# Performance work log

Hardware: AMD Instinct MI355X
Metric: run time of the kernel (lower is better)

The kernel has to match this reference:

```python
import jax, jax.numpy as jnp
from jax import lax
import numpy as np

CHUNK = 64


def short_conv(x, w):
    # depthwise causal conv1d: x (B,L,D), w (D,K)
    L = x.shape[1]
    K = w.shape[1]
    xp = jnp.pad(x, ((0, 0), (K - 1, 0), (0, 0)))
    return sum(xp[:, j:j + L, :] * w[:, j] for j in range(K))


def o2b_weighted_delta_rule(k, q, v, b):
    # k,q,v,b: (B,L,H,D) float32, zero initial state
    B, L, H, D = k.shape
    C = CHUNK
    Nc = L // C

    def to_chunks(t):  # (B,L,H,D) -> (Nc,B,H,C,D)
        return t.transpose(0, 2, 1, 3).reshape(B, H, Nc, C, D).transpose(2, 0, 1, 3, 4)

    Kc, Qc, Vc, Bc = map(to_chunks, (k, q, v, b))
    eyeC = jnp.eye(C, dtype=jnp.float32)
    W0 = jnp.zeros((B, H, D, D), jnp.float32)
    Cf = float(C)

    def step(carry, xs):
        W_t, W_avg = carry
        i, Ki, Qi, Vi, Bi = xs
        KiT = jnp.swapaxes(Ki, -1, -2)
        T = jnp.tril(Bi @ KiT, k=-1)                      # (B,H,C,C) strictly lower
        inv = jnp.linalg.inv(eyeC + T)
        Ui = inv @ (Vi - Bi @ W_t)                        # (B,H,C,D)
        W_new = W_t + KiT @ Ui
        ts = (i * C).astype(jnp.float32)                  # init t == 0 for all batches
        idx = jnp.arange(1, C + 1, dtype=jnp.float32) + ts  # (C,)
        cs = jnp.cumsum(idx)
        weighted_idx = idx + idx.sum() - cs
        w_i = (weighted_idx / ((1 + ts + Cf) * (ts + Cf) / 2))[:, None]  # (C,1)
        coef1 = ts / (ts + Cf) * ((1 + ts) / (1 + ts + Cf))
        coef2 = Cf / (ts + Cf) * ((ts * 2 + 1 + Cf) / (1 + ts + Cf))
        W_avg_new = coef1 * W_avg + coef2 * W_t + KiT @ (Ui * w_i)
        tri0 = (1 + ts) * ts / 2
        a = (tri0 / (tri0 + cs))[:, None]                 # (C,1)
        c = 1.0 - a
        r = cs[:, None]                                   # (C,1)
        j_idx = (cs - idx)[None, :]                       # (1,C)
        T_mat = jnp.where(r >= j_idx, (r - j_idx) / (tri0 + r), 0.0)  # (C,C)
        O_i = (Qi @ W_avg) * a + (Qi @ W_t) * c + (T_mat * (Qi @ KiT)) @ Ui
        return (W_new, W_avg_new), O_i

    (_, _), O = lax.scan(step, (W0, W0), (jnp.arange(Nc), Kc, Qc, Vc, Bc))
    # O: (Nc,B,H,C,D) -> (B,L,H,D)
    return O.transpose(1, 2, 0, 3, 4).reshape(B, H, L, D).transpose(0, 2, 1, 3)


def setup_inputs() -> dict:
    key = jax.random.key(0)
    ks = jax.random.split(key, 9)
    B, L, Dm, H = 4, 2048, 1024, 16
    Dh, K = Dm // H, 4
    s = 0.02
    return {
        'x': jax.random.normal(ks[0], (B, L, Dm), jnp.float32),
        'Wk': s * jax.random.normal(ks[1], (Dm, Dm), jnp.float32),
        'bk': jnp.zeros((Dm,), jnp.float32),
        'Wq': s * jax.random.normal(ks[2], (Dm, Dm), jnp.float32),
        'bq': jnp.zeros((Dm,), jnp.float32),
        'Wv': s * jax.random.normal(ks[3], (Dm, Dm), jnp.float32),
        'bv': jnp.zeros((Dm,), jnp.float32),
        'Wbeta': s * jax.random.normal(ks[4], (H, Dm), jnp.float32),
        'bbeta': jnp.zeros((H,), jnp.float32),
        'conv_k': 0.1 * jax.random.normal(ks[5], (Dm, K), jnp.float32),
        'conv_q': 0.1 * jax.random.normal(ks[6], (Dm, K), jnp.float32),
        'conv_v': 0.1 * jax.random.normal(ks[7], (Dm, K), jnp.float32),
        'rms_w': jnp.ones((Dh,), jnp.float32),
        'Wout': s * jax.random.normal(ks[8], (Dm, Dm), jnp.float32),
        'bout': jnp.zeros((Dm,), jnp.float32),
    }


def reference(x, Wk, bk, Wq, bq, Wv, bv, Wbeta, bbeta, conv_k, conv_q, conv_v, rms_w, Wout, bout):
    B, L, Dm = x.shape
    H = Wbeta.shape[0]
    Dh = Dm // H
    k = short_conv(x @ Wk.T + bk, conv_k)
    q = short_conv(x @ Wq.T + bq, conv_q)
    v = short_conv(x @ Wv.T + bv, conv_v)
    beta = jax.nn.sigmoid(x @ Wbeta.T + bbeta)            # (B,L,H)
    k = k.reshape(B, L, H, Dh)
    q = q.reshape(B, L, H, Dh)
    v = jax.nn.silu(v.reshape(B, L, H, Dh))
    knorm = jnp.linalg.norm(k, axis=-1, keepdims=True)
    qnorm = jnp.linalg.norm(q, axis=-1, keepdims=True)
    k = k / (knorm + 1e-6)
    q = q / (qnorm + 1e-6)
    eta = beta  # eta coefficient = 1.0, ogd_mode='deltanet'
    b = eta[..., None] * k
    v = eta[..., None] * v
    o = o2b_weighted_delta_rule(k, q, v, b)               # (B,L,H,Dh)
    o = o * jax.lax.rsqrt(jnp.mean(o * o, axis=-1, keepdims=True) + 1e-6) * rms_w
    o = o.reshape(B, L, Dm)
    return o @ Wout.T + bout
```

## Files before the change

kernel.cpp:

```cpp
#include <hip/hip_runtime.h>

typedef __attribute__((ext_vector_type(8))) short bf16x8;
typedef __attribute__((ext_vector_type(4))) float f32x4;

#define MFMA(a, b, c) __builtin_amdgcn_mfma_f32_16x16x32_bf16((a), (b), (c), 0, 0, 0)

__device__ inline unsigned short f2bf_rne(float f) {
  unsigned int u = __float_as_uint(f);
  u += 0x7FFFu + ((u >> 16) & 1u);
  return (unsigned short)(u >> 16);
}

__global__ __launch_bounds__(256) void prepare_kernel(
    const float* __restrict__ x, const float* __restrict__ Wk,
    const float* __restrict__ Wq, const float* __restrict__ Wv,
    const float* __restrict__ Wout, const float* __restrict__ bk,
    const float* __restrict__ bq, const float* __restrict__ bv,
    unsigned short* __restrict__ x16, unsigned short* __restrict__ wk16,
    unsigned short* __restrict__ wq16, unsigned short* __restrict__ wv16,
    unsigned short* __restrict__ wo16, float* __restrict__ b3) {
  const int gid = blockIdx.x * 256 + threadIdx.x;
  const int stride = gridDim.x * 256;
  for (int i = gid; i < 2097152; i += stride) {
    const float4 v = ((const float4*)x)[i];
    ushort4 o = {f2bf_rne(v.x), f2bf_rne(v.y), f2bf_rne(v.z), f2bf_rne(v.w)};
    ((ushort4*)x16)[i] = o;
  }
  for (int i = gid; i < 262144; i += stride) {
    float4 v = ((const float4*)Wk)[i];
    ushort4 o = {f2bf_rne(v.x), f2bf_rne(v.y), f2bf_rne(v.z), f2bf_rne(v.w)};
    ((ushort4*)wk16)[i] = o;
    v = ((const float4*)Wq)[i];
    o = (ushort4){f2bf_rne(v.x), f2bf_rne(v.y), f2bf_rne(v.z), f2bf_rne(v.w)};
    ((ushort4*)wq16)[i] = o;
    v = ((const float4*)Wv)[i];
    o = (ushort4){f2bf_rne(v.x), f2bf_rne(v.y), f2bf_rne(v.z), f2bf_rne(v.w)};
    ((ushort4*)wv16)[i] = o;
    v = ((const float4*)Wout)[i];
    o = (ushort4){f2bf_rne(v.x), f2bf_rne(v.y), f2bf_rne(v.z), f2bf_rne(v.w)};
    ((ushort4*)wo16)[i] = o;
  }
  if (gid < 3072)
    b3[gid] = gid < 1024 ? bk[gid] : gid < 2048 ? bq[gid - 1024] : bv[gid - 2048];
// ... 117 lines not shown
    const float4 wq4 = *(const float4*)(convq + (size_t)c * 4);
    const float4 wv4 = *(const float4*)(convv + (size_t)c * 4);
    const float wk[4] = {wk4.x, wk4.y, wk4.z, wk4.w};
    const float wq[4] = {wq4.x, wq4.y, wq4.z, wq4.w};
    const float wvv[4] = {wv4.x, wv4.y, wv4.z, wv4.w};
    float kc = 0.f, qc = 0.f, vc = 0.f;
#pragma unroll
    for (int jj = 0; jj < 4; ++jj) {
      const int lj = l - 3 + jj;
      if (lj >= 0) {
        const size_t rb = (size_t)(m - l + lj) * 3072 + c;
        kc += wk[jj] * qkv[rb];
        qc += wq[jj] * qkv[rb + 1024];
        vc += wvv[jj] * qkv[rb + 2048];
      }
    }
    float ssk = kc * kc, ssq = qc * qc;
    ssk += __shfl_xor(ssk, 1); ssq += __shfl_xor(ssq, 1);
    ssk += __shfl_xor(ssk, 2); ssq += __shfl_xor(ssq, 2);
    ssk += __shfl_xor(ssk, 4); ssq += __shfl_xor(ssq, 4);
    ssk += __shfl_xor(ssk, 8); ssq += __shfl_xor(ssq, 8);
    ssk += __shfl_xor(ssk, 16); ssq += __shfl_xor(ssq, 16);
    ssk += __shfl_xor(ssk, 32); ssq += __shfl_xor(ssq, 32);
    const float eta = etas_sm[h];
    const size_t o = (size_t)m * 1024 + c;
    kn16[o] = f2bf_rne(kc / (sqrtf(ssk) + 1e-6f));
    qn16[o] = f2bf_rne(qc / (sqrtf(ssq) + 1e-6f));
    vz[o] = eta * vc / (1.f + expf(-vc));
  }
}

#define LDB 72

__global__ __launch_bounds__(512, 1) void scan_kernel(
    const unsigned short* __restrict__ kn16, const unsigned short* __restrict__ qn16,
    const float* __restrict__ vz, const float* __restrict__ betab,
    float* __restrict__ O) {
  __shared__ unsigned short Kb[2][64 * LDB], Qb[2][64 * LDB], Ktb[64 * LDB];
  __shared__ unsigned short Wtb[64 * LDB], Wavgtb[64 * LDB];
  __shared__ unsigned short Pb[2][64 * LDB], Ptb[2][64 * LDB], Ztb[2][64 * LDB];
  __shared__ unsigned short P1b[64 * LDB], Utwb[64 * LDB];

  const int tid = threadIdx.x;
  const int bh = blockIdx.x;
  const int b = bh >> 4, h = bh & 15;
  const int wv = tid >> 6, lane = tid & 63;
  const int fr = lane & 15, og = lane >> 4;
  const int i0 = (wv >> 2) * 2, i1 = i0 + 1, j = wv & 3;
  const int gcol = j * 16 + fr;
  const int row0 = i0 * 16 + og * 4;
  const int row1 = i1 * 16 + og * 4;

  for (int t = tid; t < 64 * LDB; t += 512) { Wtb[t] = 0; Wavgtb[t] = 0; }

  const size_t base = ((size_t)b * 2048) * 1024 + (size_t)h * 64;
  const unsigned short* kp = kn16 + base;
  const unsigned short* qp = qn16 + base;
  const float* vp = vz + base;
  const float* etap = betab + (size_t)b * 2048 * 16 + h;
  float* Op = O + (size_t)bh * 2048 * 64;

  f32x4 Wt[2], Wav[2];
  Wt[0] = Wt[1] = Wav[0] = Wav[1] = (f32x4){0.f, 0.f, 0.f, 0.f};

  const int sr = tid >> 3, sc8 = (tid & 7) * 8;

  {
    const size_t g = (size_t)sr * 1024 + sc8;
    *(ushort4*)&Kb[0][sr * LDB + sc8] = *(const ushort4*)(kp + g);
    *(ushort4*)&Kb[0][sr * LDB + sc8 + 4] = *(const ushort4*)(kp + g + 4);
    *(ushort4*)&Qb[0][sr * LDB + sc8] = *(const ushort4*)(qp + g);
    *(ushort4*)&Qb[0][sr * LDB + sc8 + 4] = *(const ushort4*)(qp + g + 4);
    ushort4 t0v, t1v;
    t0v.x = kp[(size_t)(sc8 + 0) * 1024 + sr];
    t0v.y = kp[(size_t)(sc8 + 1) * 1024 + sr];
    t0v.z = kp[(size_t)(sc8 + 2) * 1024 + sr];
    t0v.w = kp[(size_t)(sc8 + 3) * 1024 + sr];
    t1v.x = kp[(size_t)(sc8 + 4) * 1024 + sr];
    t1v.y = kp[(size_t)(sc8 + 5) * 1024 + sr];
    t1v.z = kp[(size_t)(sc8 + 6) * 1024 + sr];
    t1v.w = kp[(size_t)(sc8 + 7) * 1024 + sr];
    *(ushort4*)&Ktb[sr * LDB + sc8] = t0v;
    *(ushort4*)&Ktb[sr * LDB + sc8 + 4] = t1v;
  }
  float vr0[4], vr1[4], er0[4], er1[4];
#pragma unroll
  for (int r = 0; r < 4; ++r) {
    vr0[r] = vp[(size_t)(row0 + r) * 1024 + gcol];
    vr1[r] = vp[(size_t)(row1 + r) * 1024 + gcol];
    er0[r] = etap[(size_t)(row0 + r) * 16];
    er1[r] = etap[(size_t)(row1 + r) * 16];
  }
  ushort4 pk0, pk1, pq0, pq1, pt0, pt1;
  __syncthreads();

#pragma unroll 1
  for (int ic = 0; ic < 32; ++ic) {
    const int cur = ic & 1, nxt = cur ^ 1;
    const float ts = (float)(ic * 64);
    const int icn = (ic < 31) ? ic + 1 : ic;

    f32x4 Zacc[2], RHSs[2];
    {
      if (ic > 0) {
        *(ushort4*)&Ktb[sr * LDB + sc8] = pt0;
        *(ushort4*)&Ktb[sr * LDB + sc8 + 4] = pt1;
      }
      const size_t gn = (size_t)(icn * 64 + sr) * 1024 + sc8;
      pk0 = *(const ushort4*)(kp + gn);
      pk1 = *(const ushort4*)(kp + gn + 4);
      pq0 = *(const ushort4*)(qp + gn);
      pq1 = *(const ushort4*)(qp + gn + 4);
      {
        const size_t cb = (size_t)(icn * 64 + sc8);
        pt0.x = kp[(cb + 0) * 1024 + sr]; pt0.y = kp[(cb + 1) * 1024 + sr];
        pt0.z = kp[(cb + 2) * 1024 + sr]; pt0.w = kp[(cb + 3) * 1024 + sr];
        pt1.x = kp[(cb + 4) * 1024 + sr]; pt1.y = kp[(cb + 5) * 1024 + sr];
        pt1.z = kp[(cb + 6) * 1024 + sr]; pt1.w = kp[(cb + 7) * 1024 + sr];
      }
      bf16x8 aK0[2], aK1[2], bK[2], bW[2];
#pragma unroll
      for (int t = 0; t < 2; ++t) {
        aK0[t] = *(const bf16x8*)&Kb[cur][(i0 * 16 + fr) * LDB + t * 32 + og * 8];
        aK1[t] = *(const bf16x8*)&Kb[cur][(i1 * 16 + fr) * LDB + t * 32 + og * 8];
        bK[t] = *(const bf16x8*)&Kb[cur][(j * 16 + fr) * LDB + t * 32 + og * 8];
        bW[t] = *(const bf16x8*)&Wtb[(j * 16 + fr) * LDB + t * 32 + og * 8];
      }
      f32x4 accT0 = {0, 0, 0, 0}, accT1 = {0, 0, 0, 0};
      f32x4 accR0 = {0, 0, 0, 0}, accR1 = {0, 0, 0, 0};
#pragma unroll
      for (int t = 0; t < 2; ++t) {
        accT0 = MFMA(aK0[t], bK[t], accT0);
        accT1 = MFMA(aK1[t], bK[t], accT1);
        accR0 = MFMA(aK0[t], bW[t], accR0);
        accR1 = MFMA(aK1[t], bW[t], accR1);
      }
#pragma unroll
      for (int s = 0; s < 2; ++s) {
        const int rb = s ? row1 : row0;
        const f32x4 aT = s ? accT1 : accT0;
        const f32x4 aR = s ? accR1 : accR0;
        unsigned short us[4];
        float zv[4];
#pragma unroll
        for (int r = 0; r < 4; ++r) {
          const int grow = rb + r;
          const float eta = s ? er1[r] : er0[r];
          const float vv = s ? vr1[r] : vr0[r];
          const float tvv = (gcol < grow) ? -eta * aT[r] : 0.f;
          us[r] = f2bf_rne(tvv);
          zv[r] = vv - eta * aR[r];
          Pb[0][grow * LDB + gcol] = us[r];
          P1b[grow * LDB + gcol] = us[r];
        }
        ushort4 pp = {us[0], us[1], us[2], us[3]};
        *(ushort4*)&Ptb[0][gcol * LDB + rb] = pp;
        ushort4 zp = {f2bf_rne(zv[0]), f2bf_rne(zv[1]), f2bf_rne(zv[2]), f2bf_rne(zv[3])};
        *(ushort4*)&Ztb[0][gcol * LDB + rb] = zp;
        Zacc[s] = (f32x4){zv[0], zv[1], zv[2], zv[3]};
        RHSs[s] = Zacc[s];
      }
    }
    __syncthreads();

#pragma unroll
    for (int k = 0; k < 6; ++k) {
      const int pc = k & 1, pn = pc ^ 1;
      bf16x8 aP0[2], aP1[2], bZ[2];
#pragma unroll
      for (int t = 0; t < 2; ++t) {
        aP0[t] = *(const bf16x8*)&Pb[pc][(i0 * 16 + fr) * LDB + t * 32 + og * 8];
        aP1[t] = *(const bf16x8*)&Pb[pc][(i1 * 16 + fr) * LDB + t * 32 + og * 8];
        bZ[t] = *(const bf16x8*)&Ztb[pc][(j * 16 + fr) * LDB + t * 32 + og * 8];
      }
      f32x4 sq0 = {0, 0, 0, 0}, sq1 = {0, 0, 0, 0};
      if (k < 5) {
#pragma unroll
        for (int t = 0; t < 2; ++t) {
          bf16x8 bPt = *(const bf16x8*)&Ptb[pc][(j * 16 + fr) * LDB + t * 32 + og * 8];
          sq0 = MFMA(aP0[t], bPt, sq0);
          sq1 = MFMA(aP1[t], bPt, sq1);
        }
      }
#pragma unroll
      for (int t = 0; t < 2; ++t) {
        Zacc[0] = MFMA(aP0[t], bZ[t], Zacc[0]);
        Zacc[1] = MFMA(aP1[t], bZ[t], Zacc[1]);
      }
#pragma unroll
      for (int s = 0; s < 2; ++s) {
        const int rb = s ? row1 : row0;
        const f32x4 zz = Zacc[s];
        ushort4 zp = {f2bf_rne(zz[0]), f2bf_rne(zz[1]), f2bf_rne(zz[2]), f2bf_rne(zz[3])};
        *(ushort4*)&Ztb[pn][gcol * LDB + rb] = zp;
        if (k < 5) {
          const f32x4 sv = s ? sq1 : sq0;
          unsigned short u0 = f2bf_rne(sv[0]), u1 = f2bf_rne(sv[1]);
          unsigned short u2 = f2bf_rne(sv[2]), u3 = f2bf_rne(sv[3]);
          Pb[pn][(rb + 0) * LDB + gcol] = u0;
          Pb[pn][(rb + 1) * LDB + gcol] = u1;
          Pb[pn][(rb + 2) * LDB + gcol] = u2;
          Pb[pn][(rb + 3) * LDB + gcol] = u3;
          ushort4 pp = {u0, u1, u2, u3};
          *(ushort4*)&Ptb[pn][gcol * LDB + rb] = pp;
        }
      }
      __syncthreads();
    }

    bf16x8 a0[2], a1[2];
    {
      *(ushort4*)&Kb[nxt][sr * LDB + sc8] = pk0;
      *(ushort4*)&Kb[nxt][sr * LDB + sc8 + 4] = pk1;
      *(ushort4*)&Qb[nxt][sr * LDB + sc8] = pq0;
      *(ushort4*)&Qb[nxt][sr * LDB + sc8 + 4] = pq1;
#pragma unroll
      for (int t = 0; t < 2; ++t) {
        a0[t] = *(const bf16x8*)&P1b[(i0 * 16 + fr) * LDB + t * 32 + og * 8];
        a1[t] = *(const bf16x8*)&P1b[(i1 * 16 + fr) * LDB + t * 32 + og * 8];
      }
      f32x4 R0 = RHSs[0] - Zacc[0];
      f32x4 R1 = RHSs[1] - Zacc[1];
#pragma unroll
      for (int t = 0; t < 2; ++t) {
        bf16x8 bU = *(const bf16x8*)&Ztb[0][(j * 16 + fr) * LDB + t * 32 + og * 8];
        R0 = MFMA(a0[t], bU, R0);
        R1 = MFMA(a1[t], bU, R1);
      }
      ushort4 r0p = {f2bf_rne(R0[0]), f2bf_rne(R0[1]), f2bf_rne(R0[2]), f2bf_rne(R0[3])};
      ushort4 r1p = {f2bf_rne(R1[0]), f2bf_rne(R1[1]), f2bf_rne(R1[2]), f2bf_rne(R1[3])};
      *(ushort4*)&Pb[1][gcol * LDB + row0] = r0p;
      *(ushort4*)&Pb[1][gcol * LDB + row1] = r1p;
      RHSs[0] = R0;
      RHSs[1] = R1;
    }
    __syncthreads();

    {
      f32x4 dU0 = RHSs[0], dU1 = RHSs[1];
#pragma unroll
      for (int t = 0; t < 2; ++t) {
        bf16x8 bR = *(const bf16x8*)&Pb[1][(j * 16 + fr) * LDB + t * 32 + og * 8];
        dU0 = MFMA(a0[t], bR, dU0);
        dU1 = MFMA(a1[t], bR, dU1);
      }
      Zacc[0] += dU0;
      Zacc[1] += dU1;
#pragma unroll
      for (int r = 0; r < 4; ++r) {
        vr0[r] = vp[(size_t)(icn * 64 + row0 + r) * 1024 + gcol];
        vr1[r] = vp[(size_t)(icn * 64 + row1 + r) * 1024 + gcol];
        er0[r] = etap[(size_t)(icn * 64 + row0 + r) * 16];
        er1[r] = etap[(size_t)(icn * 64 + row1 + r) * 16];
      }
      const float invden = 1.f / (0.5f * (ts + 65.f) * (ts + 64.f));
#pragma unroll
      for (int s = 0; s < 2; ++s) {
        const int rb = s ? row1 : row0;
        const f32x4 uu = Zacc[s];
        ushort4 up = {f2bf_rne(uu[0]), f2bf_rne(uu[1]), f2bf_rne(uu[2]), f2bf_rne(uu[3])};
        *(ushort4*)&Ztb[0][gcol * LDB + rb] = up;
        unsigned short uw[4];
#pragma unroll
        for (int r = 0; r < 4; ++r) {
          const float rr = (float)(rb + r);
          const float wr = (ts * (64.f - rr) + (rr + 1.f) + 2080.f -
                            0.5f * (rr + 1.f) * (rr + 2.f)) * invden;
          uw[r] = f2bf_rne(uu[r] * wr);
        }
        ushort4 uwp = {uw[0], uw[1], uw[2], uw[3]};
        *(ushort4*)&Utwb[gcol * LDB + rb] = uwp;
      }
    }
    f32x4 Oacc[2];
    {
      bf16x8 aQ0[2], aQ1[2], bKj[2], bWt2[2], bWa2[2];
#pragma unroll
      for (int t = 0; t < 2; ++t) {
        aQ0[t] = *(const bf16x8*)&Qb[cur][(i0 * 16 + fr) * LDB + t * 32 + og * 8];
        aQ1[t] = *(const bf16x8*)&Qb[cur][(i1 * 16 + fr) * LDB + t * 32 + og * 8];
        bKj[t] = *(const bf16x8*)&Kb[cur][(j * 16 + fr) * LDB + t * 32 + og * 8];
        bWt2[t] = *(const bf16x8*)&Wtb[(j * 16 + fr) * LDB + t * 32 + og * 8];
        bWa2[t] = *(const bf16x8*)&Wavgtb[(j * 16 + fr) * LDB + t * 32 + og * 8];
      }
      f32x4 aS0 = {0, 0, 0, 0}, aS1 = {0, 0, 0, 0};
      f32x4 aA0 = {0, 0, 0, 0}, aA1 = {0, 0, 0, 0};
      f32x4 aC0 = {0, 0, 0, 0}, aC1 = {0, 0, 0, 0};
#pragma unroll
      for (int t = 0; t < 2; ++t) {
        aS0 = MFMA(aQ0[t], bKj[t], aS0);
        aS1 = MFMA(aQ1[t], bKj[t], aS1);
        aA0 = MFMA(aQ0[t], bWa2[t], aA0);
        aA1 = MFMA(aQ1[t], bWa2[t], aA1);
        aC0 = MFMA(aQ0[t], bWt2[t], aC0);
        aC1 = MFMA(aQ1[t], bWt2[t], aC1);
      }
      const float tri0 = 0.5f * ts * (ts + 1.f);
      const float jidx = gcol * ts + 0.5f * gcol * (gcol + 1.f);
#pragma unroll
      for (int s = 0; s < 2; ++s) {
        const int rb = s ? row1 : row0;
        const f32x4 sS = s ? aS1 : aS0;
        const f32x4 sA = s ? aA1 : aA0;
        const f32x4 sC = s ? aC1 : aC0;
        f32x4 oo;
#pragma unroll
        for (int r = 0; r < 4; ++r) {
          const float grow = (float)(rb + r);
          const float csr = (grow + 1.f) * ts + 0.5f * (grow + 1.f) * (grow + 2.f);
          const float rinv = 1.f / (tri0 + csr);
          const float av = tri0 * rinv;
          oo[r] = av * sA[r] + (1.f - av) * sC[r];
          const float svv = (csr >= jidx) ? (csr - jidx) * rinv * sS[r] : 0.f;
          Ptb[1][(rb + r) * LDB + gcol] = f2bf_rne(svv);
        }
        Oacc[s] = oo;
      }
    }
    __syncthreads();

    {
      bf16x8 aS0[2], aS1[2], bU2[2];
#pragma unroll
      for (int t = 0; t < 2; ++t) {
        aS0[t] = *(const bf16x8*)&Ptb[1][(i0 * 16 + fr) * LDB + t * 32 + og * 8];
        aS1[t] = *(const bf16x8*)&Ptb[1][(i1 * 16 + fr) * LDB + t * 32 + og * 8];
        bU2[t] = *(const bf16x8*)&Ztb[0][(j * 16 + fr) * LDB + t * 32 + og * 8];
      }
#pragma unroll
      for (int t = 0; t < 2; ++t) {
        Oacc[0] = MFMA(aS0[t], bU2[t], Oacc[0]);
        Oacc[1] = MFMA(aS1[t], bU2[t], Oacc[1]);
      }
#pragma unroll
      for (int s = 0; s < 2; ++s) {
        const int rb = s ? row1 : row0;
#pragma unroll
        for (int r = 0; r < 4; ++r)
          Op[(size_t)(ic * 64 + rb + r) * 64 + gcol] = Oacc[s][r];
      }
    }

    {
      bf16x8 aU0[2], aU1[2], aW0[2], aW1[2], bKt2[2];
#pragma unroll
      for (int t = 0; t < 2; ++t) {
        aU0[t] = *(const bf16x8*)&Ztb[0][(i0 * 16 + fr) * LDB + t * 32 + og * 8];
        aU1[t] = *(const bf16x8*)&Ztb[0][(i1 * 16 + fr) * LDB + t * 32 + og * 8];
        aW0[t] = *(const bf16x8*)&Utwb[(i0 * 16 + fr) * LDB + t * 32 + og * 8];
        aW1[t] = *(const bf16x8*)&Utwb[(i1 * 16 + fr) * LDB + t * 32 + og * 8];
        bKt2[t] = *(const bf16x8*)&Ktb[(j * 16 + fr) * LDB + t * 32 + og * 8];
      }
      const float den = (ts + 64.f) * (ts + 65.f);
      const float cc1 = ts * (ts + 1.f) / den;
      const float cc2 = 64.f * (2.f * ts + 65.f) / den;
      f32x4 wn0 = cc1 * Wav[0] + cc2 * Wt[0];
      f32x4 wn1 = cc1 * Wav[1] + cc2 * Wt[1];
#pragma unroll
      for (int t = 0; t < 2; ++t) {
        wn0 = MFMA(aW0[t], bKt2[t], wn0);
        wn1 = MFMA(aW1[t], bKt2[t], wn1);
        Wt[0] = MFMA(aU0[t], bKt2[t], Wt[0]);
        Wt[1] = MFMA(aU1[t], bKt2[t], Wt[1]);
      }
      Wav[0] = wn0;
      Wav[1] = wn1;
#pragma unroll
      for (int s = 0; s < 2; ++s) {
        const int rb = s ? row1 : row0;
        const f32x4 wtv = Wt[s];
        const f32x4 wav2 = Wav[s];
#pragma unroll
        for (int r = 0; r < 4; ++r) {
          Wtb[(rb + r) * LDB + gcol] = f2bf_rne(wtv[r]);
          Wavgtb[(rb + r) * LDB + gcol] = f2bf_rne(wav2[r]);
        }
      }
    }
    __syncthreads();
  }
}

__global__ __launch_bounds__(256) void rms_kernel(const float* __restrict__ O,
                                                  const float* __restrict__ rmsw,
                                                  unsigned short* __restrict__ out16) {
  const int m = blockIdx.x;
  const int b = m >> 11, l = m & 2047;
  const int wv = threadIdx.x >> 6, lane = threadIdx.x & 63;
  const float rw = rmsw[lane];
#pragma unroll
  for (int hh = 0; hh < 4; ++hh) {
    const int h = wv * 4 + hh;
    const float v = O[(((size_t)(b * 16 + h)) * 2048 + l) * 64 + lane];
    float ss = v * v;
    ss += __shfl_xor(ss, 1); ss += __shfl_xor(ss, 2); ss += __shfl_xor(ss, 4);
    ss += __shfl_xor(ss, 8); ss += __shfl_xor(ss, 16); ss += __shfl_xor(ss, 32);
    const float sc = rsqrtf(ss * (1.f / 64.f) + 1e-6f);
    out16[(size_t)m * 1024 + h * 64 + lane] = f2bf_rne(v * sc * rw);
  }
}

extern "C" void kernel_launch(void* const* d_in, const int* in_sizes, int n_in,
                              void* d_out, int out_size, void* d_ws, size_t ws_size,
                              hipStream_t stream) {
  (void)in_sizes; (void)n_in; (void)out_size; (void)ws_size;
  const float* x     = (const float*)d_in[0];
  const float* Wk    = (const float*)d_in[1];
  const float* bk    = (const float*)d_in[2];
  const float* Wq    = (const float*)d_in[3];
  const float* bq    = (const float*)d_in[4];
  const float* Wv    = (const float*)d_in[5];
  const float* bv    = (const float*)d_in[6];
  const float* Wbeta = (const float*)d_in[7];
  const float* bbeta = (const float*)d_in[8];
  const float* convk = (const float*)d_in[9];
  const float* convq = (const float*)d_in[10];
  const float* convv = (const float*)d_in[11];
  const float* rmsw  = (const float*)d_in[12];
  const float* Wout  = (const float*)d_in[13];
  const float* bout  = (const float*)d_in[14];
  float* out = (float*)d_out;
  float* ws = (float*)d_ws;

  const size_t SZ = (size_t)8192 * 1024;
  float* qkv = ws;
  float* betab = ws + 3 * SZ;
  unsigned short* x16 = (unsigned short*)(ws + 3 * SZ + 131072);
  unsigned short* wk16 = x16 + SZ;
  unsigned short* wq16 = wk16 + 1048576;
  unsigned short* wv16 = wq16 + 1048576;
  unsigned short* wo16 = wv16 + 1048576;
  unsigned short* kn16 = wo16 + 1048576;
  unsigned short* qn16 = kn16 + SZ;
  float* b3 = (float*)(qn16 + SZ);
  float* vzb = out;
  float* Obuf = qkv;
  unsigned short* normed16 = (unsigned short*)(ws + SZ);

  dim3 blk(256);
  hipLaunchKernelGGL(prepare_kernel, dim3(2048), blk, 0, stream, x, Wk, Wq, Wv, Wout,
                     bk, bq, bv, x16, wk16, wq16, wv16, wo16, b3);
  hipLaunchKernelGGL(gemm_bf16_nt, dim3(64, 24), blk, 0, stream, x16, wk16, b3,
                     qkv, 8192, 3072, 1024);
  hipLaunchKernelGGL(prep_kernel, dim3(8192), blk, 0, stream, x, qkv, Wbeta, bbeta,
                     convk, convq, convv, betab, kn16, qn16, vzb);
  hipLaunchKernelGGL(scan_kernel, dim3(64), dim3(512), 0, stream, kn16, qn16, vzb,
                     betab, Obuf);
  hipLaunchKernelGGL(rms_kernel, dim3(8192), blk, 0, stream, Obuf, rmsw, normed16);
  hipLaunchKernelGGL(gemm_bf16_nt, dim3(64, 8), blk, 0, stream, normed16, wo16, bout, out,
                     8192, 1024, 1024);
}
```

Before: 546.0 us.

## Split chunked delta-rule scan into parallel per-chunk precompute and lean sequential scan

Moves all state-independent per-chunk work (the triangular inverse applied to V and to eta*K, plus the causal Q·K^T weighting matrix) out of the sequential scan into a new kernel launched over all 2048 chunk tiles. That kernel writes G = -(I+T)^-1 B, S, and Y = (I+T)^-1 V to global memory. The 64-block scan then only does the state-dependent MFMAs per chunk: U = Y + G·W, the outputs and the W updates. This shortens the serial critical path at the cost of an extra launch, extra global traffic for the intermediates and a reshuffled workspace layout.

```diff
diff --git a/kernel.cpp b/kernel.cpp
--- a/kernel.cpp
+++ b/kernel.cpp
@@ -9,6 +9,9 @@
   unsigned int u = __float_as_uint(f);
   u += 0x7FFFu + ((u >> 16) & 1u);
   return (unsigned short)(u >> 16);
+}
+__device__ inline float bf2f(unsigned short u) {
+  return __uint_as_float(((unsigned int)u) << 16);
 }
 
 __global__ __launch_bounds__(256) void prepare_kernel(
@@ -192,14 +195,240 @@
 
 #define LDB 72
 
-__global__ __launch_bounds__(512, 1) void scan_kernel(
+__global__ __launch_bounds__(512, 1) void chunk_kernel(
     const unsigned short* __restrict__ kn16, const unsigned short* __restrict__ qn16,
     const float* __restrict__ vz, const float* __restrict__ betab,
-    float* __restrict__ O) {
-  __shared__ unsigned short Kb[2][64 * LDB], Qb[2][64 * LDB], Ktb[64 * LDB];
+    unsigned short* __restrict__ Gg, unsigned short* __restrict__ Sg,
+    float* __restrict__ Yg) {
+  __shared__ unsigned short Kb[64 * LDB], Qb[64 * LDB], P1b[64 * LDB];
+  __shared__ unsigned short Pb[2][64 * LDB], Ptb[2][64 * LDB];
+  __shared__ unsigned short ZYb[2][64 * LDB], ZG0b[64 * LDB];
+  unsigned short* const ZG[2] = {ZG0b, Kb};
+  unsigned short* const Sb = Qb;
+
+  const int tid = threadIdx.x;
+  const int tile = blockIdx.x, bh = tile >> 5, ic = tile & 31;
+  const int b = bh >> 4, h = bh & 15;
+  const float ts = (float)(ic * 64);
+  const int wv = tid >> 6, lane = tid & 63;
+  const int fr = lane & 15, og = lane >> 4;
+  const int i0 = (wv >> 2) * 2, i1 = i0 + 1, j = wv & 3;
+  const int gcol = j * 16 + fr;
+  const int row0 = i0 * 16 + og * 4;
+  const int row1 = i1 * 16 + og * 4;
+  const int sr = tid >> 3, sc8 = (tid & 7) * 8;
+
+  const size_t base = ((size_t)b * 2048) * 1024 + (size_t)h * 64;
+  const unsigned short* kp = kn16 + base;
+  const unsigned short* qp = qn16 + base;
+  const float* vp = vz + base;
+  const float* etap = betab + (size_t)b * 2048 * 16 + h;
+
+  {
+    const size_t g = (size_t)(ic * 64 + sr) * 1024 + sc8;
+    *(ushort4*)&Kb[sr * LDB + sc8] = *(const ushort4*)(kp + g);
+    *(ushort4*)&Kb[sr * LDB + sc8 + 4] = *(const ushort4*)(kp + g + 4);
+    *(ushort4*)&Qb[sr * LDB + sc8] = *(const ushort4*)(qp + g);
+    *(ushort4*)&Qb[sr * LDB + sc8 + 4] = *(const ushort4*)(qp + g + 4);
+  }
+  float vr0[4], vr1[4], er0[4], er1[4];
+#pragma unroll
+  for (int r = 0; r < 4; ++r) {
+    vr0[r] = vp[(size_t)(ic * 64 + row0 + r) * 1024 + gcol];
+    vr1[r] = vp[(size_t)(ic * 64 + row1 + r) * 1024 + gcol];
+    er0[r] = etap[(size_t)(ic * 64 + row0 + r) * 16];
+    er1[r] = etap[(size_t)(ic * 64 + row1 + r) * 16];
+  }
+  __syncthreads();
+
+  f32x4 ZaccY[2], ZaccG[2], sSv[2];
+  float G0s[2][4];
+  {
+    bf16x8 aK0[2], aK1[2], aQ0[2], aQ1[2], bK[2];
+#pragma unroll
+    for (int t = 0; t < 2; ++t) {
+      aK0[t] = *(const bf16x8*)&Kb[(i0 * 16 + fr) * LDB + t * 32 + og * 8];
+      aK1[t] = *(const bf16x8*)&Kb[(i1 * 16 + fr) * LDB + t * 32 + og * 8];
+      aQ0[t] = *(const bf16x8*)&Qb[(i0 * 16 + fr) * LDB + t * 32 + og * 8];
+      aQ1[t] = *(const bf16x8*)&Qb[(i1 * 16 + fr) * LDB + t * 32 + og * 8];
+      bK[t] = *(const bf16x8*)&Kb[(j * 16 + fr) * LDB + t * 32 + og * 8];
+    }
+    f32x4 accT0 = {0, 0, 0, 0}, accT1 = {0, 0, 0, 0};
+    f32x4 accS0 = {0, 0, 0, 0}, accS1 = {0, 0, 0, 0};
+#pragma unroll
+    for (int t = 0; t < 2; ++t) {
+      accT0 = MFMA(aK0[t], bK[t], accT0);
+      accT1 = MFMA(aK1[t], bK[t], accT1);
+      accS0 = MFMA(aQ0[t], bK[t], accS0);
+      accS1 = MFMA(aQ1[t], bK[t], accS1);
+    }
+    const float tri0 = 0.5f * ts * (ts + 1.f);
+    const float jidx = gcol * ts + 0.5f * gcol * (gcol + 1.f);
+#pragma unroll
+    for (int s = 0; s < 2; ++s) {
+      const int rb = s ? row1 : row0;
+      const f32x4 aT = s ? accT1 : accT0;
+      const f32x4 aS = s ? accS1 : accS0;
+      unsigned short us[4];
+      f32x4 sv;
+#pragma unroll
+      for (int r = 0; r < 4; ++r) {
+        const int grow = rb + r;
+        const float eta = s ? er1[r] : er0[r];
+        const float tvv = (gcol < grow) ? -eta * aT[r] : 0.f;
+        us[r] = f2bf_rne(tvv);
+        Pb[0][grow * LDB + gcol] = us[r];
+        P1b[grow * LDB + gcol] = us[r];
+        const float csr = (grow + 1.f) * ts + 0.5f * (grow + 1.f) * (grow + 2.f);
+        const float rinv = 1.f / (tri0 + csr);
+        sv[r] = (csr >= jidx) ? (csr - jidx) * rinv * aS[r] : 0.f;
+        const float kv = bf2f(Kb[grow * LDB + gcol]);
+        G0s[s][r] = eta * kv;
+      }
+      sSv[s] = sv;
+      ushort4 pp = {us[0], us[1], us[2], us[3]};
+      *(ushort4*)&Ptb[0][gcol * LDB + rb] = pp;
+      const float* vr = s ? vr1 : vr0;
+      ZaccY[s] = (f32x4){vr[0], vr[1], vr[2], vr[3]};
+      ushort4 yp = {f2bf_rne(vr[0]), f2bf_rne(vr[1]), f2bf_rne(vr[2]), f2bf_rne(vr[3])};
+      *(ushort4*)&ZYb[0][gcol * LDB + rb] = yp;
+      ZaccG[s] = (f32x4){G0s[s][0], G0s[s][1], G0s[s][2], G0s[s][3]};
+      ushort4 gp = {f2bf_rne(G0s[s][0]), f2bf_rne(G0s[s][1]),
+                    f2bf_rne(G0s[s][2]), f2bf_rne(G0s[s][3])};
+      *(ushort4*)&ZG[0][gcol * LDB + rb] = gp;
+    }
+  }
+  __syncthreads();
+
+#pragma unroll
+  for (int k = 0; k < 6; ++k) {
+    const int pc = k & 1, pn = pc ^ 1;
+    bf16x8 aP0[2], aP1v[2], bZy[2], bZg[2];
+#pragma unroll
+    for (int t = 0; t < 2; ++t) {
+      aP0[t] = *(const bf16x8*)&Pb[pc][(i0 * 16 + fr) * LDB + t * 32 + og * 8];
+      aP1v[t] = *(const bf16x8*)&Pb[pc][(i1 * 16 + fr) * LDB + t * 32 + og * 8];
+      bZy[t] = *(const bf16x8*)&ZYb[pc][(j * 16 + fr) * LDB + t * 32 + og * 8];
+      bZg[t] = *(const bf16x8*)&ZG[pc][(j * 16 + fr) * LDB + t * 32 + og * 8];
+    }
+    f32x4 sq0 = {0, 0, 0, 0}, sq1 = {0, 0, 0, 0};
+    if (k < 5) {
+#pragma unroll
+      for (int t = 0; t < 2; ++t) {
+        bf16x8 bPt = *(const bf16x8*)&Ptb[pc][(j * 16 + fr) * LDB + t * 32 + og * 8];
+        sq0 = MFMA(aP0[t], bPt, sq0);
+        sq1 = MFMA(aP1v[t], bPt, sq1);
+      }
+    }
+#pragma unroll
+    for (int t = 0; t < 2; ++t) {
+      ZaccY[0] = MFMA(aP0[t], bZy[t], ZaccY[0]);
+      ZaccY[1] = MFMA(aP1v[t], bZy[t], ZaccY[1]);
+      ZaccG[0] = MFMA(aP0[t], bZg[t], ZaccG[0]);
+      ZaccG[1] = MFMA(aP1v[t], bZg[t], ZaccG[1]);
+    }
+#pragma unroll
+    for (int s = 0; s < 2; ++s) {
+      const int rb = s ? row1 : row0;
+      if (k == 0) {
+#pragma unroll
+        for (int r = 0; r < 4; ++r) Sb[(rb + r) * LDB + gcol] = f2bf_rne(sSv[s][r]);
+      }
+      const f32x4 zy = ZaccY[s];
+      ushort4 yp = {f2bf_rne(zy[0]), f2bf_rne(zy[1]), f2bf_rne(zy[2]), f2bf_rne(zy[3])};
+      *(ushort4*)&ZYb[pn][gcol * LDB + rb] = yp;
+      const f32x4 zg = ZaccG[s];
+      ushort4 gp = {f2bf_rne(zg[0]), f2bf_rne(zg[1]), f2bf_rne(zg[2]), f2bf_rne(zg[3])};
+      *(ushort4*)&ZG[pn][gcol * LDB + rb] = gp;
+      if (k < 5) {
+        const f32x4 sv = s ? sq1 : sq0;
+        unsigned short u0 = f2bf_rne(sv[0]), u1 = f2bf_rne(sv[1]);
+        unsigned short u2 = f2bf_rne(sv[2]), u3 = f2bf_rne(sv[3]);
+        Pb[pn][(rb + 0) * LDB + gcol] = u0;
+        Pb[pn][(rb + 1) * LDB + gcol] = u1;
+        Pb[pn][(rb + 2) * LDB + gcol] = u2;
+        Pb[pn][(rb + 3) * LDB + gcol] = u3;
+        ushort4 pp = {u0, u1, u2, u3};
+        *(ushort4*)&Ptb[pn][gcol * LDB + rb] = pp;
+      }
+    }
+    __syncthreads();
+  }
+
+  bf16x8 a10[2], a11[2];
+  f32x4 RY[2], RG[2];
+  {
+#pragma unroll
+    for (int t = 0; t < 2; ++t) {
+      a10[t] = *(const bf16x8*)&P1b[(i0 * 16 + fr) * LDB + t * 32 + og * 8];
+      a11[t] = *(const bf16x8*)&P1b[(i1 * 16 + fr) * LDB + t * 32 + og * 8];
+    }
+    RY[0] = (f32x4){vr0[0], vr0[1], vr0[2], vr0[3]} - ZaccY[0];
+    RY[1] = (f32x4){vr1[0], vr1[1], vr1[2], vr1[3]} - ZaccY[1];
+    RG[0] = (f32x4){G0s[0][0], G0s[0][1], G0s[0][2], G0s[0][3]} - ZaccG[0];
+    RG[1] = (f32x4){G0s[1][0], G0s[1][1], G0s[1][2], G0s[1][3]} - ZaccG[1];
+#pragma unroll
+    for (int t = 0; t < 2; ++t) {
+      bf16x8 bY = *(const bf16x8*)&ZYb[0][(j * 16 + fr) * LDB + t * 32 + og * 8];
+      bf16x8 bG = *(const bf16x8*)&ZG[0][(j * 16 + fr) * LDB + t * 32 + og * 8];
+      RY[0] = MFMA(a10[t], bY, RY[0]);
+      RY[1] = MFMA(a11[t], bY, RY[1]);
+      RG[0] = MFMA(a10[t], bG, RG[0]);
+      RG[1] = MFMA(a11[t], bG, RG[1]);
+    }
+#pragma unroll
+    for (int s = 0; s < 2; ++s) {
+      const int rb = s ? row1 : row0;
+      ushort4 ryp = {f2bf_rne(RY[s][0]), f2bf_rne(RY[s][1]), f2bf_rne(RY[s][2]), f2bf_rne(RY[s][3])};
+      *(ushort4*)&ZYb[1][gcol * LDB + rb] = ryp;
+      ushort4 rgp = {f2bf_rne(RG[s][0]), f2bf_rne(RG[s][1]), f2bf_rne(RG[s][2]), f2bf_rne(RG[s][3])};
+      *(ushort4*)&ZG[1][gcol * LDB + rb] = rgp;
+    }
+  }
+  __syncthreads();
+
+  {
+    f32x4 dY0 = RY[0], dY1 = RY[1], dG0 = RG[0], dG1 = RG[1];
+#pragma unroll
+    for (int t = 0; t < 2; ++t) {
+      bf16x8 bRY = *(const bf16x8*)&ZYb[1][(j * 16 + fr) * LDB + t * 32 + og * 8];
+      bf16x8 bRG = *(const bf16x8*)&ZG[1][(j * 16 + fr) * LDB + t * 32 + og * 8];
+      dY0 = MFMA(a10[t], bRY, dY0);
+      dY1 = MFMA(a11[t], bRY, dY1);
+      dG0 = MFMA(a10[t], bRG, dG0);
+      dG1 = MFMA(a11[t], bRG, dG1);
+    }
+    ZaccY[0] += dY0; ZaccY[1] += dY1;
+    ZaccG[0] += dG0; ZaccG[1] += dG1;
+    float4* yo = (float4*)(Yg + (size_t)tile * 4096 + (size_t)tid * 8);
+    yo[0] = (float4){ZaccY[0][0], ZaccY[0][1], ZaccY[0][2], ZaccY[0][3]};
+    yo[1] = (float4){ZaccY[1][0], ZaccY[1][1], ZaccY[1][2], ZaccY[1][3]};
+#pragma unroll
+    for (int s = 0; s < 2; ++s) {
+      const int rb = s ? row1 : row0;
+#pragma unroll
+      for (int r = 0; r < 4; ++r)
+        Pb[0][(rb + r) * LDB + gcol] = f2bf_rne(-ZaccG[s][r]);
+    }
+  }
+  __syncthreads();
+
+  {
+    unsigned short* So = Sg + (size_t)tile * 4096 + sr * 64 + sc8;
+    unsigned short* Go = Gg + (size_t)tile * 4096 + sr * 64 + sc8;
+    *(ushort4*)So = *(const ushort4*)&Sb[sr * LDB + sc8];
+    *(ushort4*)(So + 4) = *(const ushort4*)&Sb[sr * LDB + sc8 + 4];
+    *(ushort4*)Go = *(const ushort4*)&Pb[0][sr * LDB + sc8];
+    *(ushort4*)(Go + 4) = *(const ushort4*)&Pb[0][sr * LDB + sc8 + 4];
+  }
+}
+
+__global__ __launch_bounds__(512, 1) void scan2_kernel(
+    const unsigned short* __restrict__ kn16, const unsigned short* __restrict__ qn16,
+    const unsigned short* __restrict__ Gg, const unsigned short* __restrict__ Sg,
+    const float* __restrict__ Yg, float* __restrict__ O) {
   __shared__ unsigned short Wtb[64 * LDB], Wavgtb[64 * LDB];
-  __shared__ unsigned short Pb[2][64 * LDB], Ptb[2][64 * LDB], Ztb[2][64 * LDB];
-  __shared__ unsigned short P1b[64 * LDB], Utwb[64 * LDB];
+  __shared__ unsigned short Ztb[64 * LDB], Utwb[64 * LDB], Ktb[64 * LDB];
 
   const int tid = threadIdx.x;
   const int bh = blockIdx.x;
@@ -210,27 +439,19 @@
   const int gcol = j * 16 + fr;
   const int row0 = i0 * 16 + og * 4;
   const int row1 = i1 * 16 + og * 4;
+  const int sr = tid >> 3, sc8 = (tid & 7) * 8;
 
   for (int t = tid; t < 64 * LDB; t += 512) { Wtb[t] = 0; Wavgtb[t] = 0; }
 
   const size_t base = ((size_t)b * 2048) * 1024 + (size_t)h * 64;
   const unsigned short* kp = kn16 + base;
   const unsigned short* qp = qn16 + base;
-  const float* vp = vz + base;
-  const float* etap = betab + (size_t)b * 2048 * 16 + h;
   float* Op = O + (size_t)bh * 2048 * 64;
 
   f32x4 Wt[2], Wav[2];
   Wt[0] = Wt[1] = Wav[0] = Wav[1] = (f32x4){0.f, 0.f, 0.f, 0.f};
 
-  const int sr = tid >> 3, sc8 = (tid & 7) * 8;
-
   {
-    const size_t g = (size_t)sr * 1024 + sc8;
-    *(ushort4*)&Kb[0][sr * LDB + sc8] = *(const ushort4*)(kp + g);
-    *(ushort4*)&Kb[0][sr * LDB + sc8 + 4] = *(const ushort4*)(kp + g + 4);
-    *(ushort4*)&Qb[0][sr * LDB + sc8] = *(const ushort4*)(qp + g);
-    *(ushort4*)&Qb[0][sr * LDB + sc8 + 4] = *(const ushort4*)(qp + g + 4);
     ushort4 t0v, t1v;
     t0v.x = kp[(size_t)(sc8 + 0) * 1024 + sr];
     t0v.y = kp[(size_t)(sc8 + 1) * 1024 + sr];
@@ -243,34 +464,22 @@
     *(ushort4*)&Ktb[sr * LDB + sc8] = t0v;
     *(ushort4*)&Ktb[sr * LDB + sc8 + 4] = t1v;
   }
-  float vr0[4], vr1[4], er0[4], er1[4];
-#pragma unroll
-  for (int r = 0; r < 4; ++r) {
-    vr0[r] = vp[(size_t)(row0 + r) * 1024 + gcol];
-    vr1[r] = vp[(size_t)(row1 + r) * 1024 + gcol];
-    er0[r] = etap[(size_t)(row0 + r) * 16];
-    er1[r] = etap[(size_t)(row1 + r) * 16];
-  }
-  ushort4 pk0, pk1, pq0, pq1, pt0, pt1;
+  ushort4 pt0, pt1;
   __syncthreads();
 
 #pragma unroll 1
   for (int ic = 0; ic < 32; ++ic) {
-    const int cur = ic & 1, nxt = cur ^ 1;
     const float ts = (float)(ic * 64);
     const int icn = (ic < 31) ? ic + 1 : ic;
-
-    f32x4 Zacc[2], RHSs[2];
+    const size_t tile = (size_t)bh * 32 + ic;
+    f32x4 Oacc[2];
+    bf16x8 aS[2][2];
+
     {
       if (ic > 0) {
         *(ushort4*)&Ktb[sr * LDB + sc8] = pt0;
         *(ushort4*)&Ktb[sr * LDB + sc8 + 4] = pt1;
       }
-      const size_t gn = (size_t)(icn * 64 + sr) * 1024 + sc8;
-      pk0 = *(const ushort4*)(kp + gn);
-      pk1 = *(const ushort4*)(kp + gn + 4);
-      pq0 = *(const ushort4*)(qp + gn);
-      pq1 = *(const ushort4*)(qp + gn + 4);
       {
         const size_t cb = (size_t)(icn * 64 + sc8);
         pt0.x = kp[(cb + 0) * 1024 + sr]; pt0.y = kp[(cb + 1) * 1024 + sr];
@@ -278,192 +487,49 @@
         pt1.x = kp[(cb + 4) * 1024 + sr]; pt1.y = kp[(cb + 5) * 1024 + sr];
         pt1.z = kp[(cb + 6) * 1024 + sr]; pt1.w = kp[(cb + 7) * 1024 + sr];
       }
-      bf16x8 aK0[2], aK1[2], bK[2], bW[2];
+      const unsigned short* Gt = Gg + tile * 4096;
+      const unsigned short* St = Sg + tile * 4096;
+      bf16x8 aG[2][2], aQ[2][2];
 #pragma unroll
       for (int t = 0; t < 2; ++t) {
-        aK0[t] = *(const bf16x8*)&Kb[cur][(i0 * 16 + fr) * LDB + t * 32 + og * 8];
-        aK1[t] = *(const bf16x8*)&Kb[cur][(i1 * 16 + fr) * LDB + t * 32 + og * 8];
-        bK[t] = *(const bf16x8*)&Kb[cur][(j * 16 + fr) * LDB + t * 32 + og * 8];
+        aG[0][t] = *(const bf16x8*)(Gt + (i0 * 16 + fr) * 64 + t * 32 + og * 8);
+        aG[1][t] = *(const bf16x8*)(Gt + (i1 * 16 + fr) * 64 + t * 32 + og * 8);
+        aS[0][t] = *(const bf16x8*)(St + (i0 * 16 + fr) * 64 + t * 32 + og * 8);
+        aS[1][t] = *(const bf16x8*)(St + (i1 * 16 + fr) * 64 + t * 32 + og * 8);
+        aQ[0][t] = *(const bf16x8*)(qp + (size_t)(ic * 64 + i0 * 16 + fr) * 1024 + t * 32 + og * 8);
+        aQ[1][t] = *(const bf16x8*)(qp + (size_t)(ic * 64 + i1 * 16 + fr) * 1024 + t * 32 + og * 8);
+      }
+      const float4* yp = (const float4*)(Yg + tile * 4096 + (size_t)tid * 8);
+      const float4 ya = yp[0], yb = yp[1];
+      f32x4 U0 = {ya.x, ya.y, ya.z, ya.w};
+      f32x4 U1 = {yb.x, yb.y, yb.z, yb.w};
+      f32x4 aA0 = {0, 0, 0, 0}, aA1 = {0, 0, 0, 0};
+      f32x4 aC0 = {0, 0, 0, 0}, aC1 = {0, 0, 0, 0};
+      bf16x8 bW[2], bWa[2];
+#pragma unroll
+      for (int t = 0; t < 2; ++t) {
         bW[t] = *(const bf16x8*)&Wtb[(j * 16 + fr) * LDB + t * 32 + og * 8];
-      }
-      f32x4 accT0 = {0, 0, 0, 0}, accT1 = {0, 0, 0, 0};
-      f32x4 accR0 = {0, 0, 0, 0}, accR1 = {0, 0, 0, 0};
+        bWa[t] = *(const bf16x8*)&Wavgtb[(j * 16 + fr) * LDB + t * 32 + og * 8];
+      }
 #pragma unroll
       for (int t = 0; t < 2; ++t) {
-        accT0 = MFMA(aK0[t], bK[t], accT0);
-        accT1 = MFMA(aK1[t], bK[t], accT1);
-        accR0 = MFMA(aK0[t], bW[t], accR0);
-        accR1 = MFMA(aK1[t], bW[t], accR1);
-      }
+        U0 = MFMA(aG[0][t], bW[t], U0);
+        U1 = MFMA(aG[1][t], bW[t], U1);
+        aA0 = MFMA(aQ[0][t], bWa[t], aA0);
+        aA1 = MFMA(aQ[1][t], bWa[t], aA1);
+        aC0 = MFMA(aQ[0][t], bW[t], aC0);
+        aC1 = MFMA(aQ[1][t], bW[t], aC1);
+      }
+      const float tri0 = 0.5f * ts * (ts + 1.f);
+      const float invden = 1.f / (0.5f * (ts + 65.f) * (ts + 64.f));
 #pragma unroll
       for (int s = 0; s < 2; ++s) {
         const int rb = s ? row1 : row0;
-        const f32x4 aT = s ? accT1 : accT0;
-        const f32x4 aR = s ? accR1 : accR0;
-        unsigned short us[4];
-        float zv[4];
-#pragma unroll
-        for (int r = 0; r < 4; ++r) {
-          const int grow = rb + r;
-          const float eta = s ? er1[r] : er0[r];
-          const float vv = s ? vr1[r] : vr0[r];
-          const float tvv = (gcol < grow) ? -eta * aT[r] : 0.f;
-          us[r] = f2bf_rne(tvv);
-          zv[r] = vv - eta * aR[r];
-          Pb[0][grow * LDB + gcol] = us[r];
-          P1b[grow * LDB + gcol] = us[r];
-        }
-        ushort4 pp = {us[0], us[1], us[2], us[3]};
-        *(ushort4*)&Ptb[0][gcol * LDB + rb] = pp;
-        ushort4 zp = {f2bf_rne(zv[0]), f2bf_rne(zv[1]), f2bf_rne(zv[2]), f2bf_rne(zv[3])};
-        *(ushort4*)&Ztb[0][gcol * LDB + rb] = zp;
-        Zacc[s] = (f32x4){zv[0], zv[1], zv[2], zv[3]};
-        RHSs[s] = Zacc[s];
-      }
-    }
-    __syncthreads();
-
-#pragma unroll
-    for (int k = 0; k < 6; ++k) {
-      const int pc = k & 1, pn = pc ^ 1;
-      bf16x8 aP0[2], aP1[2], bZ[2];
-#pragma unroll
-      for (int t = 0; t < 2; ++t) {
-        aP0[t] = *(const bf16x8*)&Pb[pc][(i0 * 16 + fr) * LDB + t * 32 + og * 8];
-        aP1[t] = *(const bf16x8*)&Pb[pc][(i1 * 16 + fr) * LDB + t * 32 + og * 8];
-        bZ[t] = *(const bf16x8*)&Ztb[pc][(j * 16 + fr) * LDB + t * 32 + og * 8];
-      }
-      f32x4 sq0 = {0, 0, 0, 0}, sq1 = {0, 0, 0, 0};
-      if (k < 5) {
-#pragma unroll
-        for (int t = 0; t < 2; ++t) {
-          bf16x8 bPt = *(const bf16x8*)&Ptb[pc][(j * 16 + fr) * LDB + t * 32 + og * 8];
-          sq0 = MFMA(aP0[t], bPt, sq0);
-          sq1 = MFMA(aP1[t], bPt, sq1);
-        }
-      }
-#pragma unroll
-      for (int t = 0; t < 2; ++t) {
-        Zacc[0] = MFMA(aP0[t], bZ[t], Zacc[0]);
-        Zacc[1] = MFMA(aP1[t], bZ[t], Zacc[1]);
-      }
-#pragma unroll
-      for (int s = 0; s < 2; ++s) {
-        const int rb = s ? row1 : row0;
-        const f32x4 zz = Zacc[s];
-        ushort4 zp = {f2bf_rne(zz[0]), f2bf_rne(zz[1]), f2bf_rne(zz[2]), f2bf_rne(zz[3])};
-        *(ushort4*)&Ztb[pn][gcol * LDB + rb] = zp;
-        if (k < 5) {
-          const f32x4 sv = s ? sq1 : sq0;
-          unsigned short u0 = f2bf_rne(sv[0]), u1 = f2bf_rne(sv[1]);
-          unsigned short u2 = f2bf_rne(sv[2]), u3 = f2bf_rne(sv[3]);
-          Pb[pn][(rb + 0) * LDB + gcol] = u0;
-          Pb[pn][(rb + 1) * LDB + gcol] = u1;
-          Pb[pn][(rb + 2) * LDB + gcol] = u2;
-          Pb[pn][(rb + 3) * LDB + gcol] = u3;
-          ushort4 pp = {u0, u1, u2, u3};
-          *(ushort4*)&Ptb[pn][gcol * LDB + rb] = pp;
-        }
-      }
-      __syncthreads();
-    }
-
-    bf16x8 a0[2], a1[2];
-    {
-      *(ushort4*)&Kb[nxt][sr * LDB + sc8] = pk0;
-      *(ushort4*)&Kb[nxt][sr * LDB + sc8 + 4] = pk1;
-      *(ushort4*)&Qb[nxt][sr * LDB + sc8] = pq0;
-      *(ushort4*)&Qb[nxt][sr * LDB + sc8 + 4] = pq1;
-#pragma unroll
-      for (int t = 0; t < 2; ++t) {
-        a0[t] = *(const bf16x8*)&P1b[(i0 * 16 + fr) * LDB + t * 32 + og * 8];
-        a1[t] = *(const bf16x8*)&P1b[(i1 * 16 + fr) * LDB + t * 32 + og * 8];
-      }
-      f32x4 R0 = RHSs[0] - Zacc[0];
-      f32x4 R1 = RHSs[1] - Zacc[1];
-#pragma unroll
-      for (int t = 0; t < 2; ++t) {
-        bf16x8 bU = *(const bf16x8*)&Ztb[0][(j * 16 + fr) * LDB + t * 32 + og * 8];
-        R0 = MFMA(a0[t], bU, R0);
-        R1 = MFMA(a1[t], bU, R1);
-      }
-      ushort4 r0p = {f2bf_rne(R0[0]), f2bf_rne(R0[1]), f2bf_rne(R0[2]), f2bf_rne(R0[3])};
-      ushort4 r1p = {f2bf_rne(R1[0]), f2bf_rne(R1[1]), f2bf_rne(R1[2]), f2bf_rne(R1[3])};
-      *(ushort4*)&Pb[1][gcol * LDB + row0] = r0p;
-      *(ushort4*)&Pb[1][gcol * LDB + row1] = r1p;
-      RHSs[0] = R0;
-      RHSs[1] = R1;
-    }
-    __syncthreads();
-
-    {
-      f32x4 dU0 = RHSs[0], dU1 = RHSs[1];
-#pragma unroll
-      for (int t = 0; t < 2; ++t) {
-        bf16x8 bR = *(const bf16x8*)&Pb[1][(j * 16 + fr) * LDB + t * 32 + og * 8];
-        dU0 = MFMA(a0[t], bR, dU0);
-        dU1 = MFMA(a1[t], bR, dU1);
-      }
-      Zacc[0] += dU0;
-      Zacc[1] += dU1;
-#pragma unroll
-      for (int r = 0; r < 4; ++r) {
-        vr0[r] = vp[(size_t)(icn * 64 + row0 + r) * 1024 + gcol];
-        vr1[r] = vp[(size_t)(icn * 64 + row1 + r) * 1024 + gcol];
-        er0[r] = etap[(size_t)(icn * 64 + row0 + r) * 16];
-        er1[r] = etap[(size_t)(icn * 64 + row1 + r) * 16];
-      }
-      const float invden = 1.f / (0.5f * (ts + 65.f) * (ts + 64.f));
-#pragma unroll
-      for (int s = 0; s < 2; ++s) {
-        const int rb = s ? row1 : row0;
-        const f32x4 uu = Zacc[s];
-        ushort4 up = {f2bf_rne(uu[0]), f2bf_rne(uu[1]), f2bf_rne(uu[2]), f2bf_rne(uu[3])};
-        *(ushort4*)&Ztb[0][gcol * LDB + rb] = up;
-        unsigned short uw[4];
-#pragma unroll
-        for (int r = 0; r < 4; ++r) {
-          const float rr = (float)(rb + r);
-          const float wr = (ts * (64.f - rr) + (rr + 1.f) + 2080.f -
-                            0.5f * (rr + 1.f) * (rr + 2.f)) * invden;
-          uw[r] = f2bf_rne(uu[r] * wr);
-        }
-        ushort4 uwp = {uw[0], uw[1], uw[2], uw[3]};
-        *(ushort4*)&Utwb[gcol * LDB + rb] = uwp;
-      }
-    }
-    f32x4 Oacc[2];
-    {
-      bf16x8 aQ0[2], aQ1[2], bKj[2], bWt2[2], bWa2[2];
-#pragma unroll
-      for (int t = 0; t < 2; ++t) {
-        aQ0[t] = *(const bf16x8*)&Qb[cur][(i0 * 16 + fr) * LDB + t * 32 + og * 8];
-        aQ1[t] = *(const bf16x8*)&Qb[cur][(i1 * 16 + fr) * LDB + t * 32 + og * 8];
-        bKj[t] = *(const bf16x8*)&Kb[cur][(j * 16 + fr) * LDB + t * 32 + og * 8];
-        bWt2[t] = *(const bf16x8*)&Wtb[(j * 16 + fr) * LDB + t * 32 + og * 8];
-        bWa2[t] = *(const bf16x8*)&Wavgtb[(j * 16 + fr) * LDB + t * 32 + og * 8];
-      }
-      f32x4 aS0 = {0, 0, 0, 0}, aS1 = {0, 0, 0, 0};
-      f32x4 aA0 = {0, 0, 0, 0}, aA1 = {0, 0, 0, 0};
-      f32x4 aC0 = {0, 0, 0, 0}, aC1 = {0, 0, 0, 0};
-#pragma unroll
-      for (int t = 0; t < 2; ++t) {
-        aS0 = MFMA(aQ0[t], bKj[t], aS0);
-        aS1 = MFMA(aQ1[t], bKj[t], aS1);
-        aA0 = MFMA(aQ0[t], bWa2[t], aA0);
-        aA1 = MFMA(aQ1[t], bWa2[t], aA1);
-        aC0 = MFMA(aQ0[t], bWt2[t], aC0);
-        aC1 = MFMA(aQ1[t], bWt2[t], aC1);
-      }
-      const float tri0 = 0.5f * ts * (ts + 1.f);
-      const float jidx = gcol * ts + 0.5f * gcol * (gcol + 1.f);
-#pragma unroll
-      for (int s = 0; s < 2; ++s) {
-        const int rb = s ? row1 : row0;
-        const f32x4 sS = s ? aS1 : aS0;
         const f32x4 sA = s ? aA1 : aA0;
         const f32x4 sC = s ? aC1 : aC0;
+        const f32x4 uu = s ? U1 : U0;
         f32x4 oo;
+        unsigned short uw[4];
 #pragma unroll
         for (int r = 0; r < 4; ++r) {
           const float grow = (float)(rb + r);
@@ -471,26 +537,28 @@
           const float rinv = 1.f / (tri0 + csr);
           const float av = tri0 * rinv;
           oo[r] = av * sA[r] + (1.f - av) * sC[r];
-          const float svv = (csr >= jidx) ? (csr - jidx) * rinv * sS[r] : 0.f;
-          Ptb[1][(rb + r) * LDB + gcol] = f2bf_rne(svv);
+          const float wr = (ts * (64.f - grow) + (grow + 1.f) + 2080.f -
+                            0.5f * (grow + 1.f) * (grow + 2.f)) * invden;
+          uw[r] = f2bf_rne(uu[r] * wr);
         }
         Oacc[s] = oo;
+        ushort4 up = {f2bf_rne(uu[0]), f2bf_rne(uu[1]), f2bf_rne(uu[2]), f2bf_rne(uu[3])};
+        *(ushort4*)&Ztb[gcol * LDB + rb] = up;
+        ushort4 uwp = {uw[0], uw[1], uw[2], uw[3]};
+        *(ushort4*)&Utwb[gcol * LDB + rb] = uwp;
       }
     }
     __syncthreads();
 
     {
-      bf16x8 aS0[2], aS1[2], bU2[2];
+      bf16x8 bU[2];
+#pragma unroll
+      for (int t = 0; t < 2; ++t)
+        bU[t] = *(const bf16x8*)&Ztb[(j * 16 + fr) * LDB + t * 32 + og * 8];
 #pragma unroll
       for (int t = 0; t < 2; ++t) {
-        aS0[t] = *(const bf16x8*)&Ptb[1][(i0 * 16 + fr) * LDB + t * 32 + og * 8];
-        aS1[t] = *(const bf16x8*)&Ptb[1][(i1 * 16 + fr) * LDB + t * 32 + og * 8];
-        bU2[t] = *(const bf16x8*)&Ztb[0][(j * 16 + fr) * LDB + t * 32 + og * 8];
-      }
-#pragma unroll
-      for (int t = 0; t < 2; ++t) {
-        Oacc[0] = MFMA(aS0[t], bU2[t], Oacc[0]);
-        Oacc[1] = MFMA(aS1[t], bU2[t], Oacc[1]);
+        Oacc[0] = MFMA(aS[0][t], bU[t], Oacc[0]);
+        Oacc[1] = MFMA(aS[1][t], bU[t], Oacc[1]);
       }
 #pragma unroll
       for (int s = 0; s < 2; ++s) {
@@ -499,17 +567,14 @@
         for (int r = 0; r < 4; ++r)
           Op[(size_t)(ic * 64 + rb + r) * 64 + gcol] = Oacc[s][r];
       }
-    }
-
-    {
-      bf16x8 aU0[2], aU1[2], aW0[2], aW1[2], bKt2[2];
+      bf16x8 aU0[2], aU1[2], aW0[2], aW1[2], bKt[2];
 #pragma unroll
       for (int t = 0; t < 2; ++t) {
-        aU0[t] = *(const bf16x8*)&Ztb[0][(i0 * 16 + fr) * LDB + t * 32 + og * 8];
-        aU1[t] = *(const bf16x8*)&Ztb[0][(i1 * 16 + fr) * LDB + t * 32 + og * 8];
+        aU0[t] = *(const bf16x8*)&Ztb[(i0 * 16 + fr) * LDB + t * 32 + og * 8];
+        aU1[t] = *(const bf16x8*)&Ztb[(i1 * 16 + fr) * LDB + t * 32 + og * 8];
         aW0[t] = *(const bf16x8*)&Utwb[(i0 * 16 + fr) * LDB + t * 32 + og * 8];
         aW1[t] = *(const bf16x8*)&Utwb[(i1 * 16 + fr) * LDB + t * 32 + og * 8];
-        bKt2[t] = *(const bf16x8*)&Ktb[(j * 16 + fr) * LDB + t * 32 + og * 8];
+        bKt[t] = *(const bf16x8*)&Ktb[(j * 16 + fr) * LDB + t * 32 + og * 8];
       }
       const float den = (ts + 64.f) * (ts + 65.f);
       const float cc1 = ts * (ts + 1.f) / den;
@@ -518,10 +583,10 @@
       f32x4 wn1 = cc1 * Wav[1] + cc2 * Wt[1];
 #pragma unroll
       for (int t = 0; t < 2; ++t) {
-        wn0 = MFMA(aW0[t], bKt2[t], wn0);
-        wn1 = MFMA(aW1[t], bKt2[t], wn1);
-        Wt[0] = MFMA(aU0[t], bKt2[t], Wt[0]);
-        Wt[1] = MFMA(aU1[t], bKt2[t], Wt[1]);
+        wn0 = MFMA(aW0[t], bKt[t], wn0);
+        wn1 = MFMA(aW1[t], bKt[t], wn1);
+        Wt[0] = MFMA(aU0[t], bKt[t], Wt[0]);
+        Wt[1] = MFMA(aU1[t], bKt[t], Wt[1]);
       }
       Wav[0] = wn0;
       Wav[1] = wn1;
@@ -584,6 +649,10 @@
 
   const size_t SZ = (size_t)8192 * 1024;
   float* qkv = ws;
+  float* Obuf = ws;
+  float* Yg = ws + SZ;
+  unsigned short* Gg = (unsigned short*)(ws + 2 * SZ);
+  unsigned short* Sg = Gg + SZ;
   float* betab = ws + 3 * SZ;
   unsigned short* x16 = (unsigned short*)(ws + 3 * SZ + 131072);
   unsigned short* wk16 = x16 + SZ;
@@ -594,8 +663,7 @@
   unsigned short* qn16 = kn16 + SZ;
   float* b3 = (float*)(qn16 + SZ);
   float* vzb = out;
-  float* Obuf = qkv;
-  unsigned short* normed16 = (unsigned short*)(ws + SZ);
+  unsigned short* normed16 = x16;
 
   dim3 blk(256);
   hipLaunchKernelGGL(prepare_kernel, dim3(2048), blk, 0, stream, x, Wk, Wq, Wv, Wout,
@@ -604,8 +672,10 @@
                      qkv, 8192, 3072, 1024);
   hipLaunchKernelGGL(prep_kernel, dim3(8192), blk, 0, stream, x, qkv, Wbeta, bbeta,
                      convk, convq, convv, betab, kn16, qn16, vzb);
-  hipLaunchKernelGGL(scan_kernel, dim3(64), dim3(512), 0, stream, kn16, qn16, vzb,
-                     betab, Obuf);
+  hipLaunchKernelGGL(chunk_kernel, dim3(2048), dim3(512), 0, stream, kn16, qn16, vzb,
+                     betab, Gg, Sg, Yg);
+  hipLaunchKernelGGL(scan2_kernel, dim3(64), dim3(512), 0, stream, kn16, qn16,
+                     Gg, Sg, Yg, Obuf);
   hipLaunchKernelGGL(rms_kernel, dim3(8192), blk, 0, stream, Obuf, rmsw, normed16);
   hipLaunchKernelGGL(gemm_bf16_nt, dim3(64, 8), blk, 0, stream, normed16, wo16, bout, out,
                      8192, 1024, 1024);
```

After: 529.5 us. 1.03x faster.
